# Performance work log

Measured on AMD Instinct MI355X. Metric: run time of the kernel, lower is better.

Reference implementation:

```python
import jax, jax.numpy as jnp
import numpy as np
from jax import lax


def _attention_conv(x, Wq, bq, Wk, bk, Wv, bv, head_w, p):
    # x: [B,C,H,W]; Wq/Wk/Wv: [heads, D, D] (torch Linear weight, out x in); b*: [heads, D]
    B, C, H, W = x.shape
    pad_h = (p * (1 + H // p) - H) % p
    pad_w = (p * (1 + W // p) - W) % p
    xp = jnp.pad(x, ((0, 0), (0, 0), (p + pad_h, p), (p + pad_w, p)), mode='reflect')
    num_h = (H + pad_h) // p
    num_w = (W + pad_w) // p
    # view padded image as a grid of (num_h+2) x (num_w+2) patches of size p x p
    g = xp.reshape(B, C, num_h + 2, p, num_w + 2, p)
    # 9-patch neighborhood per window (equivalent to unfold with window=3p, stride=p)
    nb = jnp.stack([g[:, :, di:di + num_h, :, dj:dj + num_w, :]
                    for di in range(3) for dj in range(3)], axis=2)  # [B,C,9,num_h,p,num_w,p]
    tokens = nb.transpose(0, 3, 5, 2, 1, 4, 6).reshape(B * num_h * num_w, 9, C * p * p)
    D = C * p * p
    q = jnp.einsum('npd,hed->nhpe', tokens, Wq) + bq[None, :, None, :]
    k = jnp.einsum('npd,hed->nhpe', tokens, Wk) + bk[None, :, None, :]
    v = jnp.einsum('npd,hed->nhpe', tokens, Wv) + bv[None, :, None, :]
    # core patch (index 4 = center of 3x3) attends to all 9 patches
    score = jnp.einsum('nhe,nhpe->nhp', q[:, :, 4, :], k) / jnp.sqrt(jnp.float32(D))
    attn = jax.nn.softmax(score, axis=-1)               # [N,heads,9]
    out = jnp.einsum('nhp,nhpe->nhe', attn, v)          # [N,heads,D]
    mixed = jnp.einsum('h,nhe->ne', head_w[0], out)     # head-weight mixing -> [N,D]
    out = mixed.reshape(B, num_h, num_w, C, p, p).transpose(0, 3, 1, 4, 2, 5)
    out = out.reshape(B, C, num_h * p, num_w * p)
    return out[:, :, pad_h:, pad_w:]


def _dehaze(x, p3, p6, p9, conv0_w, conv0_b):
    b, c, h, w = x.shape
    avg = jnp.mean((1.0 - x).reshape(b, c, -1), axis=-1, keepdims=True)  # [b,c,1]
    xg1 = jax.nn.softmax(avg, axis=-1)[..., None]                        # softmax over size-1 dim -> ones
    xg = jnp.max((x * xg1).reshape(b, 1, -1), axis=-1, keepdims=True)[..., None]  # [b,1,1,1]
    x3 = _attention_conv(x, *p3, 1)
    x6 = _attention_conv(x3, *p6, 2)
    x9 = _attention_conv(x6, *p9, 3)
    cat = jnp.concatenate([x9, x6, x3], axis=1)
    x0 = jax.nn.relu(lax.conv_general_dilated(cat, conv0_w, (1, 1), [(2, 2), (2, 2)])
                     + conv0_b[None, :, None, None])
    return jax.nn.relu(x * x0 + (xg - x0))


def setup_inputs() -> dict:
    key = jax.random.key(0)
    ks = jax.random.split(key, 12)
    inp = {'x': jax.random.uniform(ks[0], (2, 3, 384, 384), jnp.float32)}
    specs = [('3', 6, 3), ('6', 4, 12), ('9', 2, 27)]  # (stage, num_heads, D=C*p*p)
    i = 1
    for name, h, d in specs:
        for proj in ('q', 'k', 'v'):
            inp['w%s_%s' % (name, proj)] = jax.random.normal(ks[i], (h, d, d), jnp.float32) * 0.02
            inp['b%s_%s' % (name, proj)] = jnp.zeros((h, d), jnp.float32)
            i += 1
        inp['hw%s' % name] = jnp.ones((1, h), jnp.float32) / h
    inp['conv0_w'] = jax.random.normal(ks[10], (3, 9, 5, 5), jnp.float32) * 0.02
    inp['conv0_b'] = jnp.zeros((3,), jnp.float32)
    return inp


def reference(x, w3_q, b3_q, w3_k, b3_k, w3_v, b3_v, hw3,
              w6_q, b6_q, w6_k, b6_k, w6_v, b6_v, hw6,
              w9_q, b9_q, w9_k, b9_k, w9_v, b9_v, hw9,
              conv0_w, conv0_b):
    p3 = (w3_q, b3_q, w3_k, b3_k, w3_v, b3_v, hw3)
    p6 = (w6_q, b6_q, w6_k, b6_k, w6_v, b6_v, hw6)
    p9 = (w9_q, b9_q, w9_k, b9_k, w9_v, b9_v, hw9)
    return _dehaze(x, p3, p6, p9, conv0_w, conv0_b)
```

## Files before the change

### kernel.cpp

```cpp
#include <hip/hip_runtime.h>

#define HH 384
#define HWPX (HH*HH)

#define WOFF3 16
#define HS3   40
#define WOFF6 256
#define HS6   328
#define WOFF9 1568
#define HS9   1828
#define CATOFF 8192

__device__ __forceinline__ int rx(int g) {
    g = g < 0 ? -g : g;
    return g >= HH ? 2 * HH - 2 - g : g;
}
__device__ __forceinline__ float4 fma4s(float4 a, float4 w, float t) {
    a.x += w.x * t; a.y += w.y * t; a.z += w.z * t; a.w += w.w * t; return a;
}
__device__ __forceinline__ float dot4(float4 a, float4 b) {
    return a.x * b.x + a.y * b.y + a.z * b.z + a.w * b.w;
}
__device__ __forceinline__ float f4c(const float4& v, int j) {
    return j == 0 ? v.x : (j == 1 ? v.y : (j == 2 ? v.z : v.w));
}

__global__ __launch_bounds__(256) void pre_xg(
    const float* __restrict__ w3q, const float* __restrict__ b3q,
    const float* __restrict__ w3k, const float* __restrict__ b3k,
    const float* __restrict__ w3v, const float* __restrict__ b3v, const float* __restrict__ hw3,
    const float* __restrict__ w6q, const float* __restrict__ b6q,
    const float* __restrict__ w6k, const float* __restrict__ b6k,
    const float* __restrict__ w6v, const float* __restrict__ b6v, const float* __restrict__ hw6,
    const float* __restrict__ w9q, const float* __restrict__ b9q,
    const float* __restrict__ w9k, const float* __restrict__ b9k,
    const float* __restrict__ w9v, const float* __restrict__ b9v, const float* __restrict__ hw9,
    const float* __restrict__ x, float* __restrict__ ws)
{
    __shared__ float sm[4];
    const int blk = blockIdx.x;
    const int tid = threadIdx.x;

    if (blk < 12) {
        int stage = blk < 6 ? 0 : (blk < 10 ? 1 : 2);
        int h = blk - (stage == 0 ? 0 : (stage == 1 ? 6 : 10));
        const float* WQ[3] = {w3q, w6q, w9q};
        const float* BQ[3] = {b3q, b6q, b9q};
        const float* WK[3] = {w3k, w6k, w9k};
        const float* BK[3] = {b3k, b6k, b9k};
        const float* WV_[3] = {w3v, w6v, w9v};
        const float* BV[3] = {b3v, b6v, b9v};
        const float* HWp[3] = {hw3, hw6, hw9};
        const int Ds[3] = {3, 12, 27};
        const int DPs[3] = {4, 12, 32};
        const int WOFFs[3] = {WOFF3, WOFF6, WOFF9};
        const int HSs[3] = {HS3, HS6, HS9};

        const int D = Ds[stage], DP = DPs[stage];
        const float* wq = WQ[stage] + h * D * D;
        const float* bq = BQ[stage] + h * D;
        const float* wk = WK[stage] + h * D * D;
        const float* bk = BK[stage] + h * D;
        const float* wv = WV_[stage] + h * D * D;
        const float* bv = BV[stage] + h * D;
        const float hwv = HWp[stage][h];
        float* base = ws + WOFFs[stage] + h * HSs[stage];
        const float scale = rsqrtf((float)D);

        for (int i = tid; i < D * DP; i += 256) {
            int a = i / DP, b = i % DP;
            float m = 0.f;
            if (b < D) for (int e = 0; e < D; ++e) m += wk[e * D + b] * wq[e * D + a];
            base[i] = scale * m;
            float wvv = 0.f;
            if (b < D) wvv = hwv * wv[a * D + b];
            base[D * DP + i] = wvv;
        }
        for (int i = tid; i < DP; i += 256) {
            float cv = 0.f, uv = 0.f;
            if (i < D) for (int e = 0; e < D; ++e) {
                cv += bq[e] * wk[e * D + i];
                uv += wq[e * D + i] * bk[e];
            }
            base[2 * D * DP + i] = scale * cv;
            base[2 * D * DP + DP + i] = scale * uv;
            base[2 * D * DP + 2 * DP + i] = (i < D) ? hwv * bv[i] : 0.f;
        }
        if (tid == 0) {
            float s = 0.f;
            for (int e = 0; e < D; ++e) s += bq[e] * bk[e];
            base[2 * D * DP + 3 * DP] = scale * s;
        }
    } else {
        int i2 = blk - 12;
        int b = i2 / 144, chunk = i2 % 144;
        const float4* xb = (const float4*)(x + (size_t)b * 3 * HWPX + chunk * 3072);
        float m = 0.f;
        for (int j = tid; j < 768; j += 256) {
            float4 v = xb[j];
            m = fmaxf(m, fmaxf(fmaxf(v.x, v.y), fmaxf(v.z, v.w)));
        }
        for (int off = 32; off; off >>= 1)
            m = fmaxf(m, __shfl_down(m, off));
        if ((tid & 63) == 0) sm[tid >> 6] = m;
        __syncthreads();
        if (tid == 0) {
            float mm = fmaxf(fmaxf(sm[0], sm[1]), fmaxf(sm[2], sm[3]));
            atomicMax((int*)&ws[b], __float_as_int(mm));
        }
    }
}

__global__ __launch_bounds__(256) void attn3(
    const float* __restrict__ in, float* __restrict__ out,
    const float* __restrict__ wsw)
{
    constexpr int DP = 4;
    __shared__ __align__(16) float scell[324 * DP];
    __shared__ __align__(16) float sw[6 * HS3];

    const int tid = threadIdx.x;
    const int b = blockIdx.z;
    const int BWY = blockIdx.y * 16, BWX = blockIdx.x * 16;
    const float* inb = in + (size_t)b * 3 * HWPX;

    for (int i = tid; i < 240; i += 256) sw[i] = wsw[i];
    for (int i = tid; i < 972; i += 256) {
        int c = i / 324;
        int rem = i % 324;
        int cy = rem / 18, cx = rem % 18;
        int y = rx(BWY + cy - 1);
        int x = rx(BWX + cx - 1);
        scell[(cy * 18 + cx) * DP + c] = inb[c * HWPX + y * HH + x];
    }
    for (int j = tid; j < 324; j += 256) scell[j * DP + 3] = 0.f;
    __syncthreads();

    const int wx = tid & 15, wy = tid >> 4;
    const float4 t4 = *(const float4*)&scell[((wy + 1) * 18 + wx + 1) * DP];

    float m0 = 0.f, m1 = 0.f, m2 = 0.f;
#pragma unroll 1
    for (int h = 0; h < 6; ++h) {
        const float* hb = &sw[h * HS3];
        float4 qk = *(const float4*)(hb + 24);
        float su = hb[36] + dot4(*(const float4*)(hb + 28), t4);
        qk = fma4s(qk, *(const float4*)(hb + 0), t4.x);
        qk = fma4s(qk, *(const float4*)(hb + 4), t4.y);
        qk = fma4s(qk, *(const float4*)(hb + 8), t4.z);
        float den = 0.f; float4 wt = {0.f, 0.f, 0.f, 0.f};
#pragma unroll
        for (int p = 0; p < 9; ++p) {
            const int di = p / 3, dj = p % 3;
            const float4 cv = *(const float4*)&scell[((wy + di) * 18 + wx + dj) * DP];
            float e = __expf(su + dot4(qk, cv));
            den += e; wt = fma4s(wt, cv, e);
        }
        float wi = 1.f / den;
        wt.x *= wi; wt.y *= wi; wt.z *= wi; wt.w *= wi;
        m0 += hb[32] + dot4(*(const float4*)(hb + 12), wt);
        m1 += hb[33] + dot4(*(const float4*)(hb + 16), wt);
        m2 += hb[34] + dot4(*(const float4*)(hb + 20), wt);
    }
    float* outb = out + (size_t)b * 9 * HWPX;
    const int gy = BWY + wy, gx = BWX + wx;
    outb[6 * HWPX + gy * HH + gx] = m0;
    outb[7 * HWPX + gy * HH + gx] = m1;
    outb[8 * HWPX + gy * HH + gx] = m2;
}

__global__ __launch_bounds__(256) void attn6(
    const float* __restrict__ cat, float* __restrict__ catOut,
    const float* __restrict__ wsw)
{
    __shared__ __align__(16) float scell[1200];
    __shared__ __align__(16) float sw[1312];
    __shared__ float comb[3072];

    const int tid = threadIdx.x;
    const int b = blockIdx.z;
    const int BCX = blockIdx.x * 8, BCY = blockIdx.y * 8;
    const float* inb = cat + (size_t)b * 9 * HWPX + 6 * HWPX;

    for (int i = tid; i < 328; i += 256)
        ((float4*)sw)[i] = ((const float4*)wsw)[i];
    const int by0 = 2 * BCY - 2, bx0 = 2 * BCX - 2;
    for (int i = tid; i < 1200; i += 256) {
        int c = i / 400; int rem = i - c * 400;
        int row = rem / 20, col = rem % 20;
        int gy = rx(by0 + row), gx = rx(bx0 + col);
        scell[((row >> 1) * 10 + (col >> 1)) * 12 + c * 4 + (row & 1) * 2 + (col & 1)]
            = inb[c * HWPX + gy * HH + gx];
    }
    __syncthreads();

    const int h = tid >> 6, w = tid & 63;
    const int wx = w & 7, wy = w >> 3;
    const float* hb = &sw[h * HS6];

    const float4* cc4 = (const float4*)&scell[((wy + 1) * 10 + (wx + 1)) * 12];
    const float4 t40 = cc4[0], t41 = cc4[1], t42 = cc4[2];

    float4 qk0 = *(const float4*)(hb + 288);
    float4 qk1 = *(const float4*)(hb + 292);
    float4 qk2 = *(const float4*)(hb + 296);
    float su = hb[324] + dot4(*(const float4*)(hb + 300), t40)
             + dot4(*(const float4*)(hb + 304), t41)
             + dot4(*(const float4*)(hb + 308), t42);
#pragma unroll
    for (int a = 0; a < 12; ++a) {
        const float t = f4c(a < 4 ? t40 : (a < 8 ? t41 : t42), a & 3);
        const float4* Mr = (const float4*)(hb + 12 * a);
        qk0 = fma4s(qk0, Mr[0], t);
        qk1 = fma4s(qk1, Mr[1], t);
        qk2 = fma4s(qk2, Mr[2], t);
    }
    float den = 0.f;
    float4 wt0 = {0,0,0,0}, wt1 = {0,0,0,0}, wt2 = {0,0,0,0};
#pragma unroll
    for (int p = 0; p < 9; ++p) {
        const int di = p / 3, dj = p % 3;
        const float4* cp = (const float4*)&scell[((wy + di) * 10 + (wx + dj)) * 12];
        const float4 c0 = cp[0], c1 = cp[1], c2 = cp[2];
        float e = __expf(su + dot4(qk0, c0) + dot4(qk1, c1) + dot4(qk2, c2));
        den += e;
        wt0 = fma4s(wt0, c0, e);
        wt1 = fma4s(wt1, c1, e);
        wt2 = fma4s(wt2, c2, e);
    }
    const float wi = 1.f / den;
    wt0.x *= wi; wt0.y *= wi; wt0.z *= wi; wt0.w *= wi;
    wt1.x *= wi; wt1.y *= wi; wt1.z *= wi; wt1.w *= wi;
    wt2.x *= wi; wt2.y *= wi; wt2.z *= wi; wt2.w *= wi;

    float* cbp = &comb[(h * 64 + w) * 12];
#pragma unroll
    for (int e = 0; e < 12; ++e) {
        const float4* Wr = (const float4*)(hb + 144 + 12 * e);
        cbp[e] = hb[312 + e] + dot4(Wr[0], wt0) + dot4(Wr[1], wt1) + dot4(Wr[2], wt2);
    }
    __syncthreads();

    float* outb = catOut + (size_t)b * 9 * HWPX + 3 * HWPX;
    for (int i = tid; i < 768; i += 256) {
        int w2 = i / 12, e = i % 12;
        float v = comb[w2 * 12 + e] + comb[(64 + w2) * 12 + e]
                + comb[(128 + w2) * 12 + e] + comb[(192 + w2) * 12 + e];
        int c = e >> 2, r = (e >> 1) & 1, s = e & 1;
        int gy = 2 * (BCY + (w2 >> 3)) + r, gx = 2 * (BCX + (w2 & 7)) + s;
        outb[c * HWPX + gy * HH + gx] = v;
    }
}

__global__ __launch_bounds__(256) void attn9(
    const float* __restrict__ cat, float* __restrict__ catOut,
    const float* __restrict__ wsw)
{
    __shared__ __align__(16) float scell[2160];
    __shared__ __align__(16) float sw[3656];
    __shared__ float comb[1728];

    const int tid = threadIdx.x;
    const int b = blockIdx.z;
    const int BCX = blockIdx.x * 8, BCY = blockIdx.y * 4;
    const float* inb = cat + (size_t)b * 9 * HWPX + 3 * HWPX;

    for (int i = tid; i < 914; i += 256)
        ((float4*)sw)[i] = ((const float4*)wsw)[i];
    const int by0 = 3 * BCY - 3, bx0 = 3 * BCX - 3;
    for (int i = tid; i < 1620; i += 256) {
        int c = i / 540; int rem = i - c * 540;
        int row = rem / 30, col = rem % 30;
        int gy = rx(by0 + row), gx = rx(bx0 + col);
        scell[((row / 3) * 10 + (col / 3)) * 36 + c * 9 + (row % 3) * 3 + (col % 3)]
            = inb[c * HWPX + gy * HH + gx];
    }
    for (int i = tid; i < 300; i += 256) scell[(i / 5) * 36 + 27 + (i % 5)] = 0.f;
    __syncthreads();

    const int t = tid & 3, team = tid >> 2;
    const int h = team >> 5, w = team & 31;
    const int wx = w & 7, wy = w >> 3;
    const int k0 = t, k1 = t + 4;
    const float* hb = &sw[h * HS9];

    const float4* cc4 = (const float4*)&scell[((wy + 1) * 10 + (wx + 1)) * 36];
    float4 t4r[8];
#pragma unroll
    for (int k = 0; k < 8; ++k) t4r[k] = cc4[k];

    float4 qk0 = *(const float4*)(hb + 1728 + 4 * k0);
    float4 qk1 = *(const float4*)(hb + 1728 + 4 * k1);
#pragma unroll
    for (int a = 0; a < 27; ++a) {
        const float tv = f4c(t4r[a >> 2], a & 3);
        qk0 = fma4s(qk0, *(const float4*)(hb + a * 32 + 4 * k0), tv);
        qk1 = fma4s(qk1, *(const float4*)(hb + a * 32 + 4 * k1), tv);
    }
    float upart = dot4(*(const float4*)(hb + 1760 + 4 * k0), cc4[k0])
                + dot4(*(const float4*)(hb + 1760 + 4 * k1), cc4[k1]);
    const float s0v = hb[1824];

    float den = 0.f;
    float4 wt0 = {0,0,0,0}, wt1 = {0,0,0,0};
#pragma unroll
    for (int p = 0; p < 9; ++p) {
        const int di = p / 3, dj = p % 3;
        const float4* cp = (const float4*)&scell[((wy + di) * 10 + (wx + dj)) * 36];
        const float4 c0 = cp[k0], c1 = cp[k1];
        float part = upart + dot4(qk0, c0) + dot4(qk1, c1);
        part += __shfl_xor(part, 1);
        part += __shfl_xor(part, 2);
        const float e = __expf(s0v + part);
        den += e;
        wt0 = fma4s(wt0, c0, e);
        wt1 = fma4s(wt1, c1, e);
    }
    const float wi = 1.f / den;
    wt0.x *= wi; wt0.y *= wi; wt0.z *= wi; wt0.w *= wi;
    wt1.x *= wi; wt1.y *= wi; wt1.z *= wi; wt1.w *= wi;

    float* cbp = &comb[(h * 32 + w) * 27];
#pragma unroll
    for (int e = 0; e < 27; ++e) {
        float po = dot4(*(const float4*)(hb + 864 + e * 32 + 4 * k0), wt0)
                 + dot4(*(const float4*)(hb + 864 + e * 32 + 4 * k1), wt1);
        po += __shfl_xor(po, 1);
        po += __shfl_xor(po, 2);
        if (t == 0) cbp[e] = po + hb[1792 + e];
    }
    __syncthreads();

    float* outb = catOut + (size_t)b * 9 * HWPX;
    for (int i = tid; i < 864; i += 256) {
        int w2 = i / 27, e = i % 27;
        float v = comb[w2 * 27 + e] + comb[(32 + w2) * 27 + e];
        int c = e / 9, r = (e % 9) / 3, s = e % 3;
        int gy = 3 * (BCY + (w2 >> 3)) + r, gx = 3 * (BCX + (w2 & 7)) + s;
        outb[c * HWPX + gy * HH + gx] = v;
    }
}

__global__ __launch_bounds__(256) void conv_final(
    const float* __restrict__ cat, const float* __restrict__ cw,
    const float* __restrict__ cb, const float* __restrict__ x,
    const float* __restrict__ xg, float* __restrict__ out)
{
    __shared__ float tile[9][20][40];
    __shared__ float sw[678];
    const int tid = threadIdx.x;
    const int b = blockIdx.z;
    const int bx = blockIdx.x * 32, by = blockIdx.y * 16;
    const float* catb = cat + (size_t)b * 9 * HWPX;

    for (int i = tid; i < 678; i += 256) sw[i] = (i < 675) ? cw[i] : cb[i - 675];
    for (int i = tid; i < 1800; i += 256) {
        int ci = i / 200, rem = i % 200;
        int row = rem / 10, c4 = rem % 10;
        int y = by + row - 2, xx = bx - 4 + 4 * c4;
        float4 v = {0.f, 0.f, 0.f, 0.f};
        if (y >= 0 && y < HH && xx >= 0 && xx <= HH - 4)
            v = *(const float4*)&catb[ci * HWPX + y * HH + xx];
        *(float4*)&tile[ci][row][4 * c4] = v;
    }
    __syncthreads();

    const int pxx = tid & 31, py0 = (tid >> 5) * 2;
    float acc[2][3];
    acc[0][0] = acc[1][0] = sw[675];
    acc[0][1] = acc[1][1] = sw[676];
    acc[0][2] = acc[1][2] = sw[677];

#pragma unroll 1
    for (int ci = 0; ci < 9; ++ci) {
        float rv[6][5];
#pragma unroll
        for (int rr = 0; rr < 6; ++rr)
#pragma unroll
            for (int cc = 0; cc < 5; ++cc)
                rv[rr][cc] = tile[ci][py0 + rr][pxx + 2 + cc];
#pragma unroll
        for (int ky = 0; ky < 5; ++ky)
#pragma unroll
            for (int kx = 0; kx < 5; ++kx) {
                const float w0 = sw[(0 * 9 + ci) * 25 + ky * 5 + kx];
                const float w1 = sw[(1 * 9 + ci) * 25 + ky * 5 + kx];
                const float w2 = sw[(2 * 9 + ci) * 25 + ky * 5 + kx];
                const float ta = rv[ky][kx], tb = rv[ky + 1][kx];
                acc[0][0] += ta * w0; acc[0][1] += ta * w1; acc[0][2] += ta * w2;
                acc[1][0] += tb * w0; acc[1][1] += tb * w1; acc[1][2] += tb * w2;
            }
    }

    const float xgv = xg[b];
#pragma unroll
    for (int jj = 0; jj < 2; ++jj) {
        const int gy = by + py0 + jj, gx = bx + pxx;
#pragma unroll
        for (int co = 0; co < 3; ++co) {
            const float x0 = fmaxf(acc[jj][co], 0.f);
            const float xv = x[((size_t)(b * 3 + co)) * HWPX + gy * HH + gx];
            out[((size_t)(b * 3 + co)) * HWPX + gy * HH + gx] =
                fmaxf(xv * x0 + xgv - x0, 0.f);
        }
    }
}

extern "C" void kernel_launch(void* const* d_in, const int* in_sizes, int n_in,
                              void* d_out, int out_size, void* d_ws, size_t ws_size,
                              hipStream_t stream) {
    const float* x   = (const float*)d_in[0];
    const float* w3q = (const float*)d_in[1];
    const float* b3q = (const float*)d_in[2];
    const float* w3k = (const float*)d_in[3];
    const float* b3k = (const float*)d_in[4];
    const float* w3v = (const float*)d_in[5];
    const float* b3v = (const float*)d_in[6];
    const float* hw3 = (const float*)d_in[7];
    const float* w6q = (const float*)d_in[8];
    const float* b6q = (const float*)d_in[9];
    const float* w6k = (const float*)d_in[10];
    const float* b6k = (const float*)d_in[11];
    const float* w6v = (const float*)d_in[12];
    const float* b6v = (const float*)d_in[13];
    const float* hw6 = (const float*)d_in[14];
    const float* w9q = (const float*)d_in[15];
    const float* b9q = (const float*)d_in[16];
    const float* w9k = (const float*)d_in[17];
    const float* b9k = (const float*)d_in[18];
    const float* w9v = (const float*)d_in[19];
    const float* b9v = (const float*)d_in[20];
    const float* hw9 = (const float*)d_in[21];
    const float* c0w = (const float*)d_in[22];
    const float* c0b = (const float*)d_in[23];

    float* out = (float*)d_out;
    float* ws  = (float*)d_ws;
    float* cat = ws + CATOFF;

    pre_xg<<<300, 256, 0, stream>>>(
        w3q, b3q, w3k, b3k, w3v, b3v, hw3,
        w6q, b6q, w6k, b6k, w6v, b6v, hw6,
        w9q, b9q, w9k, b9k, w9v, b9v, hw9, x, ws);

    attn3<<<dim3(24, 24, 2), 256, 0, stream>>>(x, cat, ws + WOFF3);
    attn6<<<dim3(24, 24, 2), 256, 0, stream>>>(cat, cat, ws + WOFF6);
    attn9<<<dim3(16, 32, 2), 256, 0, stream>>>(cat, cat, ws + WOFF9);

    conv_final<<<dim3(12, 24, 2), 256, 0, stream>>>(cat, c0w, c0b, x, ws, out);
}
```

Measured before the change: 195.7 us.

## Split heads across threads in attn3, restructure attn9 output projection, shrink conv tiles

```diff
diff --git a/kernel.cpp b/kernel.cpp
--- a/kernel.cpp
+++ b/kernel.cpp
@@ -111,62 +111,70 @@
     }
 }
 
-__global__ __launch_bounds__(256) void attn3(
-    const float* __restrict__ in, float* __restrict__ out,
+__global__ __launch_bounds__(256) void attn3_hs(
+    const float* __restrict__ x, float* __restrict__ cat,
     const float* __restrict__ wsw)
 {
-    constexpr int DP = 4;
-    __shared__ __align__(16) float scell[324 * DP];
-    __shared__ __align__(16) float sw[6 * HS3];
+    __shared__ float sx[216];
+    __shared__ __align__(16) float sw3[240];
+    __shared__ float comb[756];
 
     const int tid = threadIdx.x;
     const int b = blockIdx.z;
-    const int BWY = blockIdx.y * 16, BWX = blockIdx.x * 16;
-    const float* inb = in + (size_t)b * 3 * HWPX;
-
-    for (int i = tid; i < 240; i += 256) sw[i] = wsw[i];
-    for (int i = tid; i < 972; i += 256) {
-        int c = i / 324;
-        int rem = i % 324;
-        int cy = rem / 18, cx = rem % 18;
-        int y = rx(BWY + cy - 1);
-        int x = rx(BWX + cx - 1);
-        scell[(cy * 18 + cx) * DP + c] = inb[c * HWPX + y * HH + x];
-    }
-    for (int j = tid; j < 324; j += 256) scell[j * DP + 3] = 0.f;
-    __syncthreads();
-
-    const int wx = tid & 15, wy = tid >> 4;
-    const float4 t4 = *(const float4*)&scell[((wy + 1) * 18 + wx + 1) * DP];
-
-    float m0 = 0.f, m1 = 0.f, m2 = 0.f;
-#pragma unroll 1
-    for (int h = 0; h < 6; ++h) {
-        const float* hb = &sw[h * HS3];
+    const int X0 = blockIdx.x * 7, Y0 = blockIdx.y * 6;
+    const float* xb = x + (size_t)b * 3 * HWPX;
+    float* catb = cat + (size_t)b * 9 * HWPX;
+
+    if (tid < 216) {
+        int c = tid / 72, rem = tid % 72;
+        int ty = rem / 9, tx = rem % 9;
+        sx[tid] = xb[c * HWPX + rx(Y0 - 1 + ty) * HH + rx(X0 - 1 + tx)];
+    }
+    if (tid < 60) ((float4*)sw3)[tid] = ((const float4*)wsw)[tid];
+    __syncthreads();
+
+    if (tid < 252) {
+        const int w = tid % 42, h = tid / 42;
+        const int wy = w / 7, wx = w % 7;
+        float4 T[9];
+#pragma unroll
+        for (int di = 0; di < 3; ++di)
+#pragma unroll
+            for (int dj = 0; dj < 3; ++dj) {
+                const int o = (wy + di) * 9 + wx + dj;
+                T[di * 3 + dj] = make_float4(sx[o], sx[72 + o], sx[144 + o], 0.f);
+            }
+        const float* hb = &sw3[h * 40];
         float4 qk = *(const float4*)(hb + 24);
-        float su = hb[36] + dot4(*(const float4*)(hb + 28), t4);
-        qk = fma4s(qk, *(const float4*)(hb + 0), t4.x);
-        qk = fma4s(qk, *(const float4*)(hb + 4), t4.y);
-        qk = fma4s(qk, *(const float4*)(hb + 8), t4.z);
+        float su = hb[36] + dot4(*(const float4*)(hb + 28), T[4]);
+        qk = fma4s(qk, *(const float4*)(hb + 0), T[4].x);
+        qk = fma4s(qk, *(const float4*)(hb + 4), T[4].y);
+        qk = fma4s(qk, *(const float4*)(hb + 8), T[4].z);
         float den = 0.f; float4 wt = {0.f, 0.f, 0.f, 0.f};
 #pragma unroll
         for (int p = 0; p < 9; ++p) {
-            const int di = p / 3, dj = p % 3;
-            const float4 cv = *(const float4*)&scell[((wy + di) * 18 + wx + dj) * DP];
-            float e = __expf(su + dot4(qk, cv));
-            den += e; wt = fma4s(wt, cv, e);
-        }
-        float wi = 1.f / den;
+            float e = __expf(su + dot4(qk, T[p]));
+            den += e; wt = fma4s(wt, T[p], e);
+        }
+        const float wi = 1.f / den;
         wt.x *= wi; wt.y *= wi; wt.z *= wi; wt.w *= wi;
-        m0 += hb[32] + dot4(*(const float4*)(hb + 12), wt);
-        m1 += hb[33] + dot4(*(const float4*)(hb + 16), wt);
-        m2 += hb[34] + dot4(*(const float4*)(hb + 20), wt);
-    }
-    float* outb = out + (size_t)b * 9 * HWPX;
-    const int gy = BWY + wy, gx = BWX + wx;
-    outb[6 * HWPX + gy * HH + gx] = m0;
-    outb[7 * HWPX + gy * HH + gx] = m1;
-    outb[8 * HWPX + gy * HH + gx] = m2;
+        float* cb = &comb[(h * 42 + w) * 3];
+        cb[0] = hb[32] + dot4(*(const float4*)(hb + 12), wt);
+        cb[1] = hb[33] + dot4(*(const float4*)(hb + 16), wt);
+        cb[2] = hb[34] + dot4(*(const float4*)(hb + 20), wt);
+    }
+    __syncthreads();
+
+    if (tid < 126) {
+        const int w = tid / 3, c = tid % 3;
+        const int gx = X0 + w % 7;
+        if (gx < HH) {
+            float v = comb[w * 3 + c];
+#pragma unroll
+            for (int h = 1; h < 6; ++h) v += comb[(h * 42 + w) * 3 + c];
+            catb[(6 + c) * HWPX + (Y0 + w / 7) * HH + gx] = v;
+        }
+    }
 }
 
 __global__ __launch_bounds__(256) void attn6(
@@ -259,6 +267,7 @@
     __shared__ __align__(16) float scell[2160];
     __shared__ __align__(16) float sw[3656];
     __shared__ float comb[1728];
+    __shared__ __align__(16) float twt[2048];
 
     const int tid = threadIdx.x;
     const int b = blockIdx.z;
@@ -320,14 +329,24 @@
     wt0.x *= wi; wt0.y *= wi; wt0.z *= wi; wt0.w *= wi;
     wt1.x *= wi; wt1.y *= wi; wt1.z *= wi; wt1.w *= wi;
 
+    float4* tw = (float4*)&twt[team * 32];
+    tw[k0] = wt0;
+    tw[k1] = wt1;
+    float4 W[7];
+#pragma unroll
+    for (int k = 0; k < 7; ++k) W[k] = tw[k];
+
     float* cbp = &comb[(h * 32 + w) * 27];
 #pragma unroll
-    for (int e = 0; e < 27; ++e) {
-        float po = dot4(*(const float4*)(hb + 864 + e * 32 + 4 * k0), wt0)
-                 + dot4(*(const float4*)(hb + 864 + e * 32 + 4 * k1), wt1);
-        po += __shfl_xor(po, 1);
-        po += __shfl_xor(po, 2);
-        if (t == 0) cbp[e] = po + hb[1792 + e];
+    for (int ei = 0; ei < 7; ++ei) {
+        const int e = t + 4 * ei;
+        if (e < 27) {
+            const float4* Wr = (const float4*)(hb + 864 + e * 32);
+            float po = hb[1792 + e];
+#pragma unroll
+            for (int k = 0; k < 7; ++k) po += dot4(Wr[k], W[k]);
+            cbp[e] = po;
+        }
     }
     __syncthreads();
 
@@ -346,17 +365,17 @@
     const float* __restrict__ cb, const float* __restrict__ x,
     const float* __restrict__ xg, float* __restrict__ out)
 {
-    __shared__ float tile[9][20][40];
+    __shared__ __align__(16) float tile[9][20][24];
     __shared__ float sw[678];
     const int tid = threadIdx.x;
     const int b = blockIdx.z;
-    const int bx = blockIdx.x * 32, by = blockIdx.y * 16;
+    const int bx = blockIdx.x * 16, by = blockIdx.y * 16;
     const float* catb = cat + (size_t)b * 9 * HWPX;
 
     for (int i = tid; i < 678; i += 256) sw[i] = (i < 675) ? cw[i] : cb[i - 675];
-    for (int i = tid; i < 1800; i += 256) {
-        int ci = i / 200, rem = i % 200;
-        int row = rem / 10, c4 = rem % 10;
+    for (int i = tid; i < 1080; i += 256) {
+        int ci = i / 120, rem = i % 120;
+        int row = rem / 6, c4 = rem % 6;
         int y = by + row - 2, xx = bx - 4 + 4 * c4;
         float4 v = {0.f, 0.f, 0.f, 0.f};
         if (y >= 0 && y < HH && xx >= 0 && xx <= HH - 4)
@@ -365,44 +384,37 @@
     }
     __syncthreads();
 
-    const int pxx = tid & 31, py0 = (tid >> 5) * 2;
-    float acc[2][3];
-    acc[0][0] = acc[1][0] = sw[675];
-    acc[0][1] = acc[1][1] = sw[676];
-    acc[0][2] = acc[1][2] = sw[677];
+    const int lx = tid & 15, ly = tid >> 4;
+    float a0 = sw[675], a1 = sw[676], a2 = sw[677];
 
 #pragma unroll 1
     for (int ci = 0; ci < 9; ++ci) {
-        float rv[6][5];
-#pragma unroll
-        for (int rr = 0; rr < 6; ++rr)
-#pragma unroll
-            for (int cc = 0; cc < 5; ++cc)
-                rv[rr][cc] = tile[ci][py0 + rr][pxx + 2 + cc];
+        float rv[5][5];
 #pragma unroll
         for (int ky = 0; ky < 5; ++ky)
 #pragma unroll
+            for (int kx = 0; kx < 5; ++kx)
+                rv[ky][kx] = tile[ci][ly + ky][lx + 2 + kx];
+#pragma unroll
+        for (int ky = 0; ky < 5; ++ky)
+#pragma unroll
             for (int kx = 0; kx < 5; ++kx) {
-                const float w0 = sw[(0 * 9 + ci) * 25 + ky * 5 + kx];
-                const float w1 = sw[(1 * 9 + ci) * 25 + ky * 5 + kx];
-                const float w2 = sw[(2 * 9 + ci) * 25 + ky * 5 + kx];
-                const float ta = rv[ky][kx], tb = rv[ky + 1][kx];
-                acc[0][0] += ta * w0; acc[0][1] += ta * w1; acc[0][2] += ta * w2;
-                acc[1][0] += tb * w0; acc[1][1] += tb * w1; acc[1][2] += tb * w2;
+                const float tv = rv[ky][kx];
+                a0 += tv * sw[(0 * 9 + ci) * 25 + ky * 5 + kx];
+                a1 += tv * sw[(1 * 9 + ci) * 25 + ky * 5 + kx];
+                a2 += tv * sw[(2 * 9 + ci) * 25 + ky * 5 + kx];
             }
     }
 
     const float xgv = xg[b];
-#pragma unroll
-    for (int jj = 0; jj < 2; ++jj) {
-        const int gy = by + py0 + jj, gx = bx + pxx;
-#pragma unroll
-        for (int co = 0; co < 3; ++co) {
-            const float x0 = fmaxf(acc[jj][co], 0.f);
-            const float xv = x[((size_t)(b * 3 + co)) * HWPX + gy * HH + gx];
-            out[((size_t)(b * 3 + co)) * HWPX + gy * HH + gx] =
-                fmaxf(xv * x0 + xgv - x0, 0.f);
-        }
+    const int gy = by + ly, gx = bx + lx;
+    float acc[3] = {a0, a1, a2};
+#pragma unroll
+    for (int co = 0; co < 3; ++co) {
+        const float x0 = fmaxf(acc[co], 0.f);
+        const float xv = x[((size_t)(b * 3 + co)) * HWPX + gy * HH + gx];
+        out[((size_t)(b * 3 + co)) * HWPX + gy * HH + gx] =
+            fmaxf(xv * x0 + xgv - x0, 0.f);
     }
 }
 
@@ -443,9 +455,9 @@
         w6q, b6q, w6k, b6k, w6v, b6v, hw6,
         w9q, b9q, w9k, b9k, w9v, b9v, hw9, x, ws);
 
-    attn3<<<dim3(24, 24, 2), 256, 0, stream>>>(x, cat, ws + WOFF3);
+    attn3_hs<<<dim3(55, 64, 2), 256, 0, stream>>>(x, cat, ws + WOFF3);
     attn6<<<dim3(24, 24, 2), 256, 0, stream>>>(cat, cat, ws + WOFF6);
     attn9<<<dim3(16, 32, 2), 256, 0, stream>>>(cat, cat, ws + WOFF9);
 
-    conv_final<<<dim3(12, 24, 2), 256, 0, stream>>>(cat, c0w, c0b, x, ws, out);
-}
+    conv_final<<<dim3(24, 24, 2), 256, 0, stream>>>(cat, c0w, c0b, x, ws, out);
+}
```

Result: slower. 208.8 us (+6.7%).
